# Kernel tuning notes

Hardware: AMD Instinct MI355X
Metric: run time of the kernel (lower is better)

## Reference

```python
import jax, jax.numpy as jnp
import numpy as np

B, N, D = 1, 2048, 512        # batch, query seq len, model dim
H, DH = 8, 64                 # heads, head dim
MEM = 512                     # cached XL memory tokens (one window segment)
KV = N + MEM                  # kv sequence length
WINDOW = 512                  # block / sliding-window size
LOOKBACK = 1                  # lookback_blocks
N_EP = 4                      # number of episodes
SCALE = DH ** -0.5


def _rope(t, pos):
    # t: [b,h,l,dh], pos: [l]  (GPT-NeoX half rotation)
    dh = t.shape[-1]
    inv_freq = 1.0 / (10000.0 ** (jnp.arange(0, dh, 2, dtype=jnp.float32) / dh))
    freqs = pos.astype(jnp.float32)[:, None] * inv_freq[None, :]   # [l, dh/2]
    freqs = jnp.concatenate([freqs, freqs], axis=-1)               # [l, dh]
    cos, sin = jnp.cos(freqs), jnp.sin(freqs)
    x1, x2 = jnp.split(t, 2, axis=-1)
    rotated = jnp.concatenate([-x2, x1], axis=-1)
    return t * cos + rotated * sin


def setup_inputs() -> dict:
    key = jax.random.key(0)
    ks = jax.random.split(key, 8)
    x = jax.random.normal(ks[0], (B, N, D), jnp.float32)
    cache_k = jax.random.normal(ks[1], (B, H, MEM, DH), jnp.float32)
    cache_v = jax.random.normal(ks[2], (B, H, MEM, DH), jnp.float32)
    episode_ids = jnp.sort(jax.random.randint(ks[3], (B, KV), 0, N_EP, dtype=jnp.int32), axis=-1)
    Wq = jax.random.normal(ks[4], (D, H * DH), jnp.float32) * 0.02
    Wkv = jax.random.normal(ks[5], (D, 2 * H * DH), jnp.float32) * 0.02
    Wg = jax.random.normal(ks[6], (D, H), jnp.float32) * 0.02
    Wo = jax.random.normal(ks[7], (H * DH, D), jnp.float32) * 0.02
    return dict(x=x, cache_k=cache_k, cache_v=cache_v, episode_ids=episode_ids,
                Wq=Wq, Wkv=Wkv, Wg=Wg, Wo=Wo)


def _xl_mask(episode_ids):
    # mirrors create_xl_mask: causal + block window with lookback + intra-episode
    offset = KV - N
    q_pos = offset + jnp.arange(N)          # [N]
    k_pos = jnp.arange(KV)                  # [KV]
    causal = q_pos[:, None] >= k_pos[None, :]
    bq = q_pos // WINDOW
    bk = k_pos // WINDOW
    block = (bq[:, None] >= bk[None, :]) & (bq[:, None] <= bk[None, :] + LOOKBACK)
    intra_ep = episode_ids[:, q_pos][:, :, None] == episode_ids[:, None, :]  # [B,N,KV]
    return (causal & block)[None] & intra_ep                                 # [B,N,KV]


def reference(x, cache_k, cache_v, episode_ids, Wq, Wkv, Wg, Wo):
    b, n, _ = x.shape
    offset = KV - N

    q = (x @ Wq).reshape(b, n, H, DH).transpose(0, 2, 1, 3)          # [b,h,n,dh]
    kv = (x @ Wkv).reshape(b, n, 2, H, DH)
    k_new = kv[:, :, 0].transpose(0, 2, 1, 3)                        # [b,h,n,dh]
    v_new = kv[:, :, 1].transpose(0, 2, 1, 3)

    k = jnp.concatenate([cache_k, k_new], axis=2)                    # [b,h,kv,dh]
    v = jnp.concatenate([cache_v, v_new], axis=2)

    q = _rope(q, offset + jnp.arange(n))
    k = _rope(k, jnp.arange(KV))

    scores = jnp.einsum('bhnd,bhmd->bhnm', q, k) * SCALE             # [b,h,n,kv]
    mask = _xl_mask(episode_ids)[:, None]                            # [b,1,n,kv]
    scores = jnp.where(mask, scores, jnp.finfo(scores.dtype).min)
    attn = jax.nn.softmax(scores, axis=-1)

    out = jnp.einsum('bhnm,bhmd->bhnd', attn, v)                     # [b,h,n,dh]

    gates = jax.nn.sigmoid(x @ Wg).transpose(0, 2, 1)[..., None]     # [b,h,n,1]
    out = out * gates

    out = out.transpose(0, 2, 1, 3).reshape(b, n, H * DH)            # merge heads
    return out @ Wo                                                  # [b,n,d]
```

## Files before the change

### kernel.cpp

```cpp
#include <hip/hip_runtime.h>
#include <math.h>

#define NQ     2048
#define DMODEL 512
#define NH     8
#define DHD    64
#define MEMT   512
#define KVT    2560
#define QSCALE 0.125f
#define NEGF   (-1e30f)

typedef unsigned short u16;
typedef __bf16 bf16x8 __attribute__((ext_vector_type(8)));
typedef float  f32x4  __attribute__((ext_vector_type(4)));
typedef u16    u16x8  __attribute__((ext_vector_type(8)));
typedef u16    u16x4  __attribute__((ext_vector_type(4)));

__device__ __forceinline__ u16 f2bf(float f) {
    union { float f; unsigned u; } v; v.f = f;
    unsigned r = (v.u + 0x7FFFu + ((v.u >> 16) & 1u)) >> 16;
    return (u16)r;
}

__global__ __launch_bounds__(256) void prep(const float* __restrict__ x,
                                            const float* __restrict__ Wq,
                                            const float* __restrict__ Wkv,
                                            const float* __restrict__ Wo,
                                            const float* __restrict__ Wg,
                                            const float* __restrict__ cache_v,
                                            u16* __restrict__ xb,
                                            u16* __restrict__ Wt,
                                            u16* __restrict__ Wot,
                                            float* __restrict__ gates,
                                            float2* __restrict__ cs,
                                            u16* __restrict__ vtb) {
    __shared__ __attribute__((aligned(16))) char smem[17408];
    int bid = blockIdx.x, tid = threadIdx.x;

    if (bid < 32) {
        int base4 = bid * 8192;
#pragma unroll
        for (int u = 0; u < 32; ++u) {
            int i4 = base4 + u * 256 + tid;
            float4 v = ((const float4*)x)[i4];
            u16x4 o4 = { f2bf(v.x), f2bf(v.y), f2bf(v.z), f2bf(v.w) };
            *(u16x4*)&xb[i4 * 4] = o4;
        }
    } else if (bid < 288) {
        float (*tile)[65] = (float(*)[65])smem;
        int tt = bid - 32;
        bool isQKV = (tt < 192);
        int tc, tr;
        if (isQKV) { tc = tt % 24; tr = tt / 24; }
        else       { tt -= 192; tc = tt & 7; tr = tt >> 3; }
        int rr = tid >> 4, c4 = (tid & 15) * 4;
#pragma unroll
        for (int u = 0; u < 4; ++u) {
            int row = u * 16 + rr;
            int k = tr * 64 + row, c = tc * 64 + c4;
            float4 v;
            if (isQKV) v = (c < 512) ? *(const float4*)&Wq[k * 512 + c]
                                     : *(const float4*)&Wkv[k * 1024 + (c - 512)];
            else       v = *(const float4*)&Wo[k * 512 + c];
            tile[row][c4 + 0] = v.x; tile[row][c4 + 1] = v.y;
            tile[row][c4 + 2] = v.z; tile[row][c4 + 3] = v.w;
        }
        __syncthreads();
#pragma unroll
        for (int u = 0; u < 4; ++u) {
            int trow = u * 16 + rr;
            u16x4 o4;
#pragma unroll
            for (int i = 0; i < 4; ++i) o4[i] = f2bf(tile[c4 + i][trow]);
            int tg = tc * 64 + trow, kg = tr * 64 + c4;
            if (isQKV) *(u16x4*)&Wt[tg * 512 + kg] = o4;
            else       *(u16x4*)&Wot[tg * 512 + kg] = o4;
        }
    } else if (bid < 320) {
#pragma unroll
        for (int kk = 0; kk < 2; ++kk) {
            int t = (bid - 288) * 512 + kk * 256 + tid;
            int n = t >> 3, hh = t & 7;
            float acc = 0.f;
            for (int k = 0; k < DMODEL; k += 4) {
                float4 xv = *(const float4*)&x[n * DMODEL + k];
                acc += xv.x * Wg[(k + 0) * NH + hh] + xv.y * Wg[(k + 1) * NH + hh]
                     + xv.z * Wg[(k + 2) * NH + hh] + xv.w * Wg[(k + 3) * NH + hh];
            }
            gates[hh * NQ + n] = 1.f / (1.f + __expf(-acc));
        }
    } else if (bid < 384) {
#pragma unroll
        for (int kk = 0; kk < 5; ++kk) {
            int idx = (bid - 320) * 1280 + kk * 256 + tid;
            int pos = idx >> 5, j = idx & 31;
            float invf = exp2f(-(float)j * (13.287712379549449f / 32.f));
            float ss, sc;
            sincosf((float)pos * invf, &ss, &sc);
            cs[idx] = make_float2(sc, ss);
        }
    } else {
        u16 (*tile)[66] = (u16(*)[66])smem;
        int uu = bid - 384;
        int tb = uu & 7, h = uu >> 3;
        int rr = tid >> 4, c4 = (tid & 15) * 4;
        int r0 = tb * 64;
#pragma unroll
        for (int u = 0; u < 4; ++u) {
            int row = u * 16 + rr;
            float4 v = *(const float4*)&cache_v[(h * MEMT + r0 + row) * DHD + c4];
            tile[row][c4 + 0] = f2bf(v.x); tile[row][c4 + 1] = f2bf(v.y);
            tile[row][c4 + 2] = f2bf(v.z); tile[row][c4 + 3] = f2bf(v.w);
        }
        __syncthreads();
#pragma unroll
        for (int u = 0; u < 4; ++u) {
            int d = u * 16 + rr;
            u16x4 o4 = { tile[c4 + 0][d], tile[c4 + 1][d], tile[c4 + 2][d], tile[c4 + 3][d] };
            *(u16x4*)&vtb[(h * DHD + d) * KVT + r0 + c4] = o4;
        }
    }
}

__global__ __launch_bounds__(256, 2) void qkv(const u16* __restrict__ xb,
                                              const u16* __restrict__ Wt,
                                              const float2* __restrict__ cs,
                                              const float* __restrict__ cache_k,
                                              u16* __restrict__ qb,
                                              u16* __restrict__ kb,
                                              u16* __restrict__ vtb) {
    __shared__ __attribute__((aligned(16))) u16 vtile[64][66];
    const int bid = blockIdx.x, tid = threadIdx.x;
    const int w = tid >> 6, lane = tid & 63;
    const int lr = lane & 15, lg = lane >> 4;

#pragma unroll 1
    for (int pass = 0; pass < 2; ++pass) {
        int u2 = pass * 512 + bid;
        if (u2 >= 832) break;
        if (u2 < 768) {
            int i = u2 >> 3;
            int bx = (u2 & 7) * 3 + (i >> 5);
            int by = i & 31;
            int rowbase = by * 64 + (w >> 1) * 32;
            int colbase = bx * 64 + (w & 1) * 16;
            f32x4 acc[2][2];
#pragma unroll
            for (int a = 0; a < 2; ++a)
#pragma unroll
                for (int b = 0; b < 2; ++b) { f32x4 z = {0.f,0.f,0.f,0.f}; acc[a][b] = z; }
            const u16* a0 = xb + (rowbase + lr) * 512 + lg * 8;
            const u16* a1 = a0 + 16 * 512;
            const u16* b0 = Wt + (colbase + lr) * 512 + lg * 8;
            const u16* b1 = b0 + 32 * 512;
#pragma unroll 4
            for (int k0 = 0; k0 < 512; k0 += 32) {
                bf16x8 fa0 = __builtin_bit_cast(bf16x8, *(const u16x8*)(a0 + k0));
                bf16x8 fa1 = __builtin_bit_cast(bf16x8, *(const u16x8*)(a1 + k0));
                bf16x8 fb0 = __builtin_bit_cast(bf16x8, *(const u16x8*)(b0 + k0));
                bf16x8 fb1 = __builtin_bit_cast(bf16x8, *(const u16x8*)(b1 + k0));
                acc[0][0] = __builtin_amdgcn_mfma_f32_16x16x32_bf16(fa0, fb0, acc[0][0], 0, 0, 0);
                acc[0][1] = __builtin_amdgcn_mfma_f32_16x16x32_bf16(fa0, fb1, acc[0][1], 0, 0, 0);
                acc[1][0] = __builtin_amdgcn_mfma_f32_16x16x32_bf16(fa1, fb0, acc[1][0], 0, 0, 0);
                acc[1][1] = __builtin_amdgcn_mfma_f32_16x16x32_bf16(fa1, fb1, acc[1][1], 0, 0, 0);
            }
            int j = (colbase & 63) + lr;
            int region = bx >> 3;
            int h = bx & 7;
            if (region == 2) {
                __syncthreads();
#pragma unroll
                for (int rt = 0; rt < 2; ++rt)
#pragma unroll
                    for (int r = 0; r < 4; ++r) {
                        int rl = (w >> 1) * 32 + rt * 16 + lg * 4 + r;
                        vtile[rl][j]      = f2bf(acc[rt][0][r]);
                        vtile[rl][j + 32] = f2bf(acc[rt][1][r]);
                    }
                __syncthreads();
                int rr = tid >> 4, c4 = (tid & 15) * 4;
#pragma unroll
                for (int u = 0; u < 4; ++u) {
                    int d = u * 16 + rr;
                    u16x4 o4 = { vtile[c4 + 0][d], vtile[c4 + 1][d], vtile[c4 + 2][d], vtile[c4 + 3][d] };
                    *(u16x4*)&vtb[(h * DHD + d) * KVT + 512 + by * 64 + c4] = o4;
                }
            } else {
#pragma unroll
                for (int rt = 0; rt < 2; ++rt)
#pragma unroll
                    for (int r = 0; r < 4; ++r) {
                        int n = rowbase + rt * 16 + lg * 4 + r;
                        float a = acc[rt][0][r], b = acc[rt][1][r];
                        float2 csv = cs[(512 + n) * 32 + j];
                        u16 e0 = f2bf(a * csv.x - b * csv.y);
                        u16 e1 = f2bf(b * csv.x + a * csv.y);
                        if (region == 0) {
                            qb[(h * NQ + n) * DHD + j]      = e0;
                            qb[(h * NQ + n) * DHD + 32 + j] = e1;
                        } else {
                            kb[(h * KVT + 512 + n) * DHD + j]      = e0;
                            kb[(h * KVT + 512 + n) * DHD + 32 + j] = e1;
                        }
                    }
            }
        } else {
            int uu = u2 - 768;
            int r0 = (uu & 7) * 64, h = uu >> 3;
#pragma unroll
            for (int u = 0; u < 8; ++u) {
                int idx = u * 256 + tid;
                int row = idx >> 5, j = idx & 31;
                int r = r0 + row;
                float a = cache_k[(h * MEMT + r) * DHD + j];
                float b = cache_k[(h * MEMT + r) * DHD + 32 + j];
                float2 csv = cs[r * 32 + j];
                kb[(h * KVT + r) * DHD + j]      = f2bf(a * csv.x - b * csv.y);
                kb[(h * KVT + r) * DHD + 32 + j] = f2bf(b * csv.x + a * csv.y);
            }
        }
    }
}

#define LOADK(BK, BEP, C0)                                                     \
  _Pragma("unroll")                                                            \
  for (int t = 0; t < 4; ++t) {                                                \
    const u16* kr = kb + ((h * KVT + (C0) + t * 16 + lr) * DHD + lg * 8);      \
    BK[t][0] = __builtin_bit_cast(bf16x8, *(const u16x8*)kr);                  \
    BK[t][1] = __builtin_bit_cast(bf16x8, *(const u16x8*)(kr + 32));           \
    BEP[t] = ep[(C0) + t * 16 + lr];                                           \
  }

#define DO_CHUNK(C0, BK, BEP, PREF, NBK, NBEP)                                 \
  {                                                                            \
    bf16x8 bV[4][2];                                                           \
    _Pragma("unroll")                                                          \
    for (int t = 0; t < 4; ++t) {                                              \
      const u16* vr = vtb + ((h * DHD + t * 16 + lr) * KVT + (C0) + lg * 8);   \
      bV[t][0] = __builtin_bit_cast(bf16x8, *(const u16x8*)vr);                \
      bV[t][1] = __builtin_bit_cast(bf16x8, *(const u16x8*)(vr + 32));         \
    }                                                                          \
    f32x4 s[4];                                                                \
    _Pragma("unroll")                                                          \
    for (int t = 0; t < 4; ++t) {                                              \
      f32x4 z = {0.f, 0.f, 0.f, 0.f};                                          \
      s[t] = __builtin_amdgcn_mfma_f32_16x16x32_bf16(aQ[0], BK[t][0], z, 0, 0, 0); \
      s[t] = __builtin_amdgcn_mfma_f32_16x16x32_bf16(aQ[1], BK[t][1], s[t], 0, 0, 0); \
    }                                                                          \
    if (PREF) { LOADK(NBK, NBEP, (C0) + 64) }                                  \
    float rmax[4] = {NEGF, NEGF, NEGF, NEGF};                                  \
    _Pragma("unroll")                                                          \
    for (int t = 0; t < 4; ++t) {                                              \
      int key = (C0) + t * 16 + lr;                                            \
      int ek = BEP[t];                                                         \
      _Pragma("unroll")                                                        \
      for (int r = 0; r < 4; ++r) {                                            \
        bool vld = (key <= qpos[r]) && (ek == epq[r]);                         \
        float sv = vld ? s[t][r] * QSCALE : NEGF;                              \
        s[t][r] = sv;                                                          \
        rmax[r] = fmaxf(rmax[r], sv);                                          \
      }                                                                        \
    }                                                                          \
    _Pragma("unroll")                                                          \
    for (int mm = 1; mm < 16; mm <<= 1) {                                      \
      _Pragma("unroll")                                                        \
      for (int r = 0; r < 4; ++r)                                              \
        rmax[r] = fmaxf(rmax[r], __shfl_xor(rmax[r], mm, 64));                 \
    }                                                                          \
    float alpha[4];                                                            \
    _Pragma("unroll")                                                          \
    for (int r = 0; r < 4; ++r) {                                              \
      float mn = fmaxf(mrun[r], rmax[r]);                                      \
      alpha[r] = __expf(mrun[r] - mn);                                         \
      mrun[r] = mn;                                                            \
      lsum[r] *= alpha[r];                                                     \
    }                                                                          \
    _Pragma("unroll")                                                          \
    for (int t = 0; t < 4; ++t)                                                \
      _Pragma("unroll")                                                        \
      for (int r = 0; r < 4; ++r) o[t][r] *= alpha[r];                         \
    float psum[4] = {0.f, 0.f, 0.f, 0.f};                                      \
    _Pragma("unroll")                                                          \
    for (int t = 0; t < 4; ++t) {                                              \
      _Pragma("unroll")                                                        \
      for (int r = 0; r < 4; ++r) {                                            \
        float sv = s[t][r];                                                    \
        float p = (sv <= -1e29f) ? 0.f : __expf(sv - mrun[r]);                 \
        psum[r] += p;                                                          \
        int qq = lg * 4 + r;                                                   \
        int kk2 = t * 16 + lr;                                                 \
        pl[qq * 64 + (kk2 ^ ((qq & 7) << 3))] = f2bf(p);                       \
      }                                                                        \
    }                                                                          \
    _Pragma("unroll")                                                          \
    for (int mm = 1; mm < 16; mm <<= 1) {                                      \
      _Pragma("unroll")                                                        \
      for (int r = 0; r < 4; ++r) psum[r] += __shfl_xor(psum[r], mm, 64);      \
    }                                                                          \
    _Pragma("unroll")                                                          \
    for (int r = 0; r < 4; ++r) lsum[r] += psum[r];                            \
    bf16x8 aP[2];                                                              \
    {                                                                          \
      int sw = (lr & 7) << 3;                                                  \
      aP[0] = __builtin_bit_cast(bf16x8, *(const u16x8*)&pl[lr * 64 + ((lg * 8) ^ sw)]);        \
      aP[1] = __builtin_bit_cast(bf16x8, *(const u16x8*)&pl[lr * 64 + ((32 + lg * 8) ^ sw)]);   \
    }                                                                          \
    _Pragma("unroll")                                                          \
    for (int t = 0; t < 4; ++t) {                                              \
      o[t] = __builtin_amdgcn_mfma_f32_16x16x32_bf16(aP[0], bV[t][0], o[t], 0, 0, 0); \
      o[t] = __builtin_amdgcn_mfma_f32_16x16x32_bf16(aP[1], bV[t][1], o[t], 0, 0, 0); \
    }                                                                          \
  }

__global__ __launch_bounds__(256, 2) void attn_mfma(const u16* __restrict__ qb,
                                                    const u16* __restrict__ kb,
                                                    const u16* __restrict__ vtb,
                                                    const float* __restrict__ gates,
                                                    const int* __restrict__ ep,
                                                    u16* __restrict__ outp) {
    __shared__ u16 plds[4][16 * 64];
    __shared__ float o_l[2][16][68];
    __shared__ float ml_l[2][2][16];

    int bid = blockIdx.x;
    int h = bid & 7;
    int q0 = (bid >> 3) * 32;
    int tid = threadIdx.x;
    int w = tid >> 6, lane = tid & 63;
    int lr = lane & 15, lg = lane >> 4;
    int qsub = w & 1, kvh = w >> 1;
    int qbase = q0 + qsub * 16;
    u16* pl = plds[w];

    bf16x8 aQ[2];
    {
        const u16* qrow = qb + ((h * NQ + qbase + lr) * DHD + lg * 8);
        aQ[0] = __builtin_bit_cast(bf16x8, *(const u16x8*)qrow);
        aQ[1] = __builtin_bit_cast(bf16x8, *(const u16x8*)(qrow + 32));
    }

    int qpos[4], epq[4];
    float gq[4];
#pragma unroll
    for (int r = 0; r < 4; ++r) {
        int q = qbase + lg * 4 + r;
        qpos[r] = 512 + q;
        epq[r] = ep[512 + q];
        gq[r] = gates[h * NQ + q];
    }

    f32x4 o[4];
    float mrun[4], lsum[4];
#pragma unroll
    for (int t = 0; t < 4; ++t) { f32x4 z = {0.f,0.f,0.f,0.f}; o[t] = z; }
#pragma unroll
    for (int r = 0; r < 4; ++r) { mrun[r] = NEGF; lsum[r] = 0.f; }

    int c_lo = q0 & ~511;
    int nch = (544 + (q0 & 511) + 63) >> 6;
    int n0 = nch >> 1;
    int my_n = kvh ? (nch - n0) : n0;
    int c0 = c_lo + (kvh ? (n0 << 6) : 0);

    bf16x8 bKA[4][2], bKB[4][2];
    int epA[4], epB[4];

    LOADK(bKA, epA, c0)
    int ci = 0;
    while (true) {
        bool more = (ci + 1 < my_n);
        DO_CHUNK(c0, bKA, epA, more, bKB, epB)
        ++ci; c0 += 64;
        if (!more) break;
        bool more2 = (ci + 1 < my_n);
        DO_CHUNK(c0, bKB, epB, more2, bKA, epA)
        ++ci; c0 += 64;
        if (!more2) break;
    }

    if (kvh == 1) {
#pragma unroll
        for (int r = 0; r < 4; ++r) {
            ml_l[qsub][0][lg * 4 + r] = mrun[r];
            ml_l[qsub][1][lg * 4 + r] = lsum[r];
        }
#pragma unroll
        for (int t = 0; t < 4; ++t)
#pragma unroll
            for (int r = 0; r < 4; ++r)
                o_l[qsub][lg * 4 + r][t * 16 + lr] = o[t][r];
    }
    __syncthreads();
    if (kvh == 0) {
#pragma unroll
        for (int r = 0; r < 4; ++r) {
            int row = lg * 4 + r;
            float m1 = ml_l[qsub][0][row], l1 = ml_l[qsub][1][row];
            float m0 = mrun[r], l0 = lsum[r];
            float mm2 = fmaxf(m0, m1);
            float f0 = (m0 <= -1e29f) ? 0.f : __expf(m0 - mm2);
            float f1 = (m1 <= -1e29f) ? 0.f : __expf(m1 - mm2);
            float lt = l0 * f0 + l1 * f1;
            float inv = gq[r] / lt;
            int q = qbase + row;
#pragma unroll
            for (int t = 0; t < 4; ++t) {
                float o1 = o_l[qsub][row][t * 16 + lr];
                outp[q * DMODEL + h * DHD + t * 16 + lr] =
                    f2bf((o[t][r] * f0 + o1 * f1) * inv);
            }
        }
    }
}

__global__ __launch_bounds__(256, 2) void outgemm(const u16* __restrict__ attnb,
                                                  const u16* __restrict__ Wot,
                                                  float* __restrict__ outf) {
    int bid = blockIdx.x, tid = threadIdx.x;
    int w = tid >> 6, lane = tid & 63;
    int lr = lane & 15, lg = lane >> 4;
    int bx = bid & 7, by = bid >> 3;
    int rowbase = by * 32 + (w >> 1) * 16;
    int colbase = bx * 64 + (w & 1) * 16;
    f32x4 acc0 = {0.f,0.f,0.f,0.f}, acc1 = {0.f,0.f,0.f,0.f};
    const u16* a0 = attnb + (rowbase + lr) * 512 + lg * 8;
    const u16* b0 = Wot + (colbase + lr) * 512 + lg * 8;
    const u16* b1 = b0 + 32 * 512;
#pragma unroll 4
    for (int k0 = 0; k0 < 512; k0 += 32) {
        bf16x8 fa  = __builtin_bit_cast(bf16x8, *(const u16x8*)(a0 + k0));
        bf16x8 fb0 = __builtin_bit_cast(bf16x8, *(const u16x8*)(b0 + k0));
        bf16x8 fb1 = __builtin_bit_cast(bf16x8, *(const u16x8*)(b1 + k0));
        acc0 = __builtin_amdgcn_mfma_f32_16x16x32_bf16(fa, fb0, acc0, 0, 0, 0);
        acc1 = __builtin_amdgcn_mfma_f32_16x16x32_bf16(fa, fb1, acc1, 0, 0, 0);
    }
#pragma unroll
    for (int r = 0; r < 4; ++r) {
        int n = rowbase + lg * 4 + r;
        outf[n * DMODEL + colbase + lr]      = acc0[r];
        outf[n * DMODEL + colbase + 32 + lr] = acc1[r];
    }
}

extern "C" void kernel_launch(void* const* d_in, const int* in_sizes, int n_in,
                              void* d_out, int out_size, void* d_ws, size_t ws_size,
                              hipStream_t stream) {
    const float* x       = (const float*)d_in[0];
    const float* cache_k = (const float*)d_in[1];
    const float* cache_v = (const float*)d_in[2];
    const int*   ep      = (const int*)  d_in[3];
    const float* Wq      = (const float*)d_in[4];
    const float* Wkv     = (const float*)d_in[5];
    const float* Wg      = (const float*)d_in[6];
    const float* Wo      = (const float*)d_in[7];
    float* out = (float*)d_out;

    u16* u = (u16*)d_ws;
    u16* x_bf    = u;
    u16* Wt      = x_bf + 1048576;
    u16* Wot     = Wt + 786432;
    u16* q_bf    = Wot + 262144;
    u16* k_bf    = q_bf + 1048576;
    u16* vT      = k_bf + 1310720;
    u16* attn_bf = vT + 1310720;
    float*  gatesw = (float*)(attn_bf + 1048576);
    float2* cs     = (float2*)(gatesw + 16384);

    prep<<<448, 256, 0, stream>>>(x, Wq, Wkv, Wo, Wg, cache_v, x_bf, Wt, Wot, gatesw, cs, vT);
    qkv<<<512, 256, 0, stream>>>(x_bf, Wt, cs, cache_k, q_bf, k_bf, vT);
    attn_mfma<<<512, 256, 0, stream>>>(q_bf, k_bf, vT, gatesw, ep, attn_bf);
    outgemm<<<512, 256, 0, stream>>>(attn_bf, Wot, out);
}
```

Before: 159.6 us.

## Shrink per-block work to launch more blocks across all four kernels

Moves the cache_k RoPE work into the prep kernel, computing sin/cos inline. Each remaining kernel is split finer: qkv runs 32-row tiles over 1536 blocks, attention uses 16 query rows per block with the KV range split four ways across waves, and the output GEMM uses 16-row tiles over 1024 blocks. Launch bounds rise to 4 blocks per CU. The goal is to fill the large GPU with more concurrent blocks and waves. In exchange it adds a 4-way softmax merge through shared memory and less register-level reuse per wave in the GEMMs.

Result: slower. 212.0 us (+32.8%).

```diff
diff --git a/kernel.cpp b/kernel.cpp
--- a/kernel.cpp
+++ b/kernel.cpp
@@ -15,6 +15,7 @@
 typedef float  f32x4  __attribute__((ext_vector_type(4)));
 typedef u16    u16x8  __attribute__((ext_vector_type(8)));
 typedef u16    u16x4  __attribute__((ext_vector_type(4)));
+typedef u16    u16x2  __attribute__((ext_vector_type(2)));
 
 __device__ __forceinline__ u16 f2bf(float f) {
     union { float f; unsigned u; } v; v.f = f;
@@ -22,19 +23,21 @@
     return (u16)r;
 }
 
-__global__ __launch_bounds__(256) void prep(const float* __restrict__ x,
-                                            const float* __restrict__ Wq,
-                                            const float* __restrict__ Wkv,
-                                            const float* __restrict__ Wo,
-                                            const float* __restrict__ Wg,
-                                            const float* __restrict__ cache_v,
-                                            u16* __restrict__ xb,
-                                            u16* __restrict__ Wt,
-                                            u16* __restrict__ Wot,
-                                            float* __restrict__ gates,
-                                            float2* __restrict__ cs,
-                                            u16* __restrict__ vtb) {
-    __shared__ __attribute__((aligned(16))) char smem[17408];
+__global__ __launch_bounds__(256, 4) void prep(const float* __restrict__ x,
+                                               const float* __restrict__ Wq,
+                                               const float* __restrict__ Wkv,
+                                               const float* __restrict__ Wo,
+                                               const float* __restrict__ Wg,
+                                               const float* __restrict__ cache_v,
+                                               const float* __restrict__ cache_k,
+                                               u16* __restrict__ xb,
+                                               u16* __restrict__ Wt,
+                                               u16* __restrict__ Wot,
+                                               float* __restrict__ gates,
+                                               float2* __restrict__ cs,
+                                               u16* __restrict__ vtb,
+                                               u16* __restrict__ kb) {
+    __shared__ __attribute__((aligned(16))) char smem[16640];
     int bid = blockIdx.x, tid = threadIdx.x;
 
     if (bid < 32) {
@@ -99,7 +102,7 @@
             sincosf((float)pos * invf, &ss, &sc);
             cs[idx] = make_float2(sc, ss);
         }
-    } else {
+    } else if (bid < 448) {
         u16 (*tile)[66] = (u16(*)[66])smem;
         int uu = bid - 384;
         int tb = uu & 7, h = uu >> 3;
@@ -119,104 +122,90 @@
             u16x4 o4 = { tile[c4 + 0][d], tile[c4 + 1][d], tile[c4 + 2][d], tile[c4 + 3][d] };
             *(u16x4*)&vtb[(h * DHD + d) * KVT + r0 + c4] = o4;
         }
-    }
-}
-
-__global__ __launch_bounds__(256, 2) void qkv(const u16* __restrict__ xb,
+    } else {
+        int uu = bid - 448;
+        int r0 = (uu & 7) * 64, h = uu >> 3;
+        int j = tid & 31;
+        float invf = exp2f(-(float)j * (13.287712379549449f / 32.f));
+#pragma unroll
+        for (int u = 0; u < 8; ++u) {
+            int idx = u * 256 + tid;
+            int row = idx >> 5;
+            int r = r0 + row;
+            float a = cache_k[(h * MEMT + r) * DHD + j];
+            float b = cache_k[(h * MEMT + r) * DHD + 32 + j];
+            float ss, sc;
+            sincosf((float)r * invf, &ss, &sc);
+            kb[(h * KVT + r) * DHD + j]      = f2bf(a * sc - b * ss);
+            kb[(h * KVT + r) * DHD + 32 + j] = f2bf(b * sc + a * ss);
+        }
+    }
+}
+
+__global__ __launch_bounds__(256, 4) void qkv(const u16* __restrict__ xb,
                                               const u16* __restrict__ Wt,
                                               const float2* __restrict__ cs,
-                                              const float* __restrict__ cache_k,
                                               u16* __restrict__ qb,
                                               u16* __restrict__ kb,
                                               u16* __restrict__ vtb) {
-    __shared__ __attribute__((aligned(16))) u16 vtile[64][66];
+    __shared__ __attribute__((aligned(16))) u16 vtile[32][66];
     const int bid = blockIdx.x, tid = threadIdx.x;
     const int w = tid >> 6, lane = tid & 63;
     const int lr = lane & 15, lg = lane >> 4;
 
-#pragma unroll 1
-    for (int pass = 0; pass < 2; ++pass) {
-        int u2 = pass * 512 + bid;
-        if (u2 >= 832) break;
-        if (u2 < 768) {
-            int i = u2 >> 3;
-            int bx = (u2 & 7) * 3 + (i >> 5);
-            int by = i & 31;
-            int rowbase = by * 64 + (w >> 1) * 32;
-            int colbase = bx * 64 + (w & 1) * 16;
-            f32x4 acc[2][2];
-#pragma unroll
-            for (int a = 0; a < 2; ++a)
-#pragma unroll
-                for (int b = 0; b < 2; ++b) { f32x4 z = {0.f,0.f,0.f,0.f}; acc[a][b] = z; }
-            const u16* a0 = xb + (rowbase + lr) * 512 + lg * 8;
-            const u16* a1 = a0 + 16 * 512;
-            const u16* b0 = Wt + (colbase + lr) * 512 + lg * 8;
-            const u16* b1 = b0 + 32 * 512;
+    int i = bid >> 3;
+    int sub = i % 3, byr = i / 3;
+    int bx = (bid & 7) * 3 + sub;
+    int rowbase = byr * 32;
+    int rfrag = rowbase + (w >> 1) * 16;
+    int colbase = bx * 64 + (w & 1) * 16;
+
+    f32x4 acc0 = {0.f,0.f,0.f,0.f}, acc1 = {0.f,0.f,0.f,0.f};
+    const u16* a0 = xb + (rfrag + lr) * 512 + lg * 8;
+    const u16* b0 = Wt + (colbase + lr) * 512 + lg * 8;
+    const u16* b1 = b0 + 32 * 512;
 #pragma unroll 4
-            for (int k0 = 0; k0 < 512; k0 += 32) {
-                bf16x8 fa0 = __builtin_bit_cast(bf16x8, *(const u16x8*)(a0 + k0));
-                bf16x8 fa1 = __builtin_bit_cast(bf16x8, *(const u16x8*)(a1 + k0));
-                bf16x8 fb0 = __builtin_bit_cast(bf16x8, *(const u16x8*)(b0 + k0));
-                bf16x8 fb1 = __builtin_bit_cast(bf16x8, *(const u16x8*)(b1 + k0));
-                acc[0][0] = __builtin_amdgcn_mfma_f32_16x16x32_bf16(fa0, fb0, acc[0][0], 0, 0, 0);
-                acc[0][1] = __builtin_amdgcn_mfma_f32_16x16x32_bf16(fa0, fb1, acc[0][1], 0, 0, 0);
-                acc[1][0] = __builtin_amdgcn_mfma_f32_16x16x32_bf16(fa1, fb0, acc[1][0], 0, 0, 0);
-                acc[1][1] = __builtin_amdgcn_mfma_f32_16x16x32_bf16(fa1, fb1, acc[1][1], 0, 0, 0);
-            }
-            int j = (colbase & 63) + lr;
-            int region = bx >> 3;
-            int h = bx & 7;
-            if (region == 2) {
-                __syncthreads();
-#pragma unroll
-                for (int rt = 0; rt < 2; ++rt)
-#pragma unroll
-                    for (int r = 0; r < 4; ++r) {
-                        int rl = (w >> 1) * 32 + rt * 16 + lg * 4 + r;
-                        vtile[rl][j]      = f2bf(acc[rt][0][r]);
-                        vtile[rl][j + 32] = f2bf(acc[rt][1][r]);
-                    }
-                __syncthreads();
-                int rr = tid >> 4, c4 = (tid & 15) * 4;
-#pragma unroll
-                for (int u = 0; u < 4; ++u) {
-                    int d = u * 16 + rr;
-                    u16x4 o4 = { vtile[c4 + 0][d], vtile[c4 + 1][d], vtile[c4 + 2][d], vtile[c4 + 3][d] };
-                    *(u16x4*)&vtb[(h * DHD + d) * KVT + 512 + by * 64 + c4] = o4;
-                }
+    for (int k0 = 0; k0 < 512; k0 += 32) {
+        bf16x8 fa  = __builtin_bit_cast(bf16x8, *(const u16x8*)(a0 + k0));
+        bf16x8 fb0 = __builtin_bit_cast(bf16x8, *(const u16x8*)(b0 + k0));
+        bf16x8 fb1 = __builtin_bit_cast(bf16x8, *(const u16x8*)(b1 + k0));
+        acc0 = __builtin_amdgcn_mfma_f32_16x16x32_bf16(fa, fb0, acc0, 0, 0, 0);
+        acc1 = __builtin_amdgcn_mfma_f32_16x16x32_bf16(fa, fb1, acc1, 0, 0, 0);
+    }
+
+    int j = (colbase & 63) + lr;
+    int region = bx >> 3;
+    int h = bx & 7;
+    if (region == 2) {
+        __syncthreads();
+#pragma unroll
+        for (int r = 0; r < 4; ++r) {
+            int rl = (w >> 1) * 16 + lg * 4 + r;
+            vtile[rl][j]      = f2bf(acc0[r]);
+            vtile[rl][j + 32] = f2bf(acc1[r]);
+        }
+        __syncthreads();
+        int rr = tid >> 4, c2 = (tid & 15) * 2;
+#pragma unroll
+        for (int u = 0; u < 4; ++u) {
+            int d = u * 16 + rr;
+            u16x2 o2 = { vtile[c2][d], vtile[c2 + 1][d] };
+            *(u16x2*)&vtb[(h * DHD + d) * KVT + 512 + rowbase + c2] = o2;
+        }
+    } else {
+#pragma unroll
+        for (int r = 0; r < 4; ++r) {
+            int n = rfrag + lg * 4 + r;
+            float a = acc0[r], b = acc1[r];
+            float2 csv = cs[(512 + n) * 32 + j];
+            u16 e0 = f2bf(a * csv.x - b * csv.y);
+            u16 e1 = f2bf(b * csv.x + a * csv.y);
+            if (region == 0) {
+                qb[(h * NQ + n) * DHD + j]      = e0;
+                qb[(h * NQ + n) * DHD + 32 + j] = e1;
             } else {
-#pragma unroll
-                for (int rt = 0; rt < 2; ++rt)
-#pragma unroll
-                    for (int r = 0; r < 4; ++r) {
-                        int n = rowbase + rt * 16 + lg * 4 + r;
-                        float a = acc[rt][0][r], b = acc[rt][1][r];
-                        float2 csv = cs[(512 + n) * 32 + j];
-                        u16 e0 = f2bf(a * csv.x - b * csv.y);
-                        u16 e1 = f2bf(b * csv.x + a * csv.y);
-                        if (region == 0) {
-                            qb[(h * NQ + n) * DHD + j]      = e0;
-                            qb[(h * NQ + n) * DHD + 32 + j] = e1;
-                        } else {
-                            kb[(h * KVT + 512 + n) * DHD + j]      = e0;
-                            kb[(h * KVT + 512 + n) * DHD + 32 + j] = e1;
-                        }
-                    }
-            }
-        } else {
-            int uu = u2 - 768;
-            int r0 = (uu & 7) * 64, h = uu >> 3;
-#pragma unroll
-            for (int u = 0; u < 8; ++u) {
-                int idx = u * 256 + tid;
-                int row = idx >> 5, j = idx & 31;
-                int r = r0 + row;
-                float a = cache_k[(h * MEMT + r) * DHD + j];
-                float b = cache_k[(h * MEMT + r) * DHD + 32 + j];
-                float2 csv = cs[r * 32 + j];
-                kb[(h * KVT + r) * DHD + j]      = f2bf(a * csv.x - b * csv.y);
-                kb[(h * KVT + r) * DHD + 32 + j] = f2bf(b * csv.x + a * csv.y);
+                kb[(h * KVT + 512 + n) * DHD + j]      = e0;
+                kb[(h * KVT + 512 + n) * DHD + 32 + j] = e1;
             }
         }
     }
@@ -312,29 +301,27 @@
     }                                                                          \
   }
 
-__global__ __launch_bounds__(256, 2) void attn_mfma(const u16* __restrict__ qb,
+__global__ __launch_bounds__(256, 4) void attn_mfma(const u16* __restrict__ qb,
                                                     const u16* __restrict__ kb,
                                                     const u16* __restrict__ vtb,
                                                     const float* __restrict__ gates,
                                                     const int* __restrict__ ep,
                                                     u16* __restrict__ outp) {
-    __shared__ u16 plds[4][16 * 64];
-    __shared__ float o_l[2][16][68];
-    __shared__ float ml_l[2][2][16];
+    __shared__ u16 plds[4][1024];
+    __shared__ float o_l[4][16][68];
+    __shared__ float ml_l[4][2][16];
 
     int bid = blockIdx.x;
     int h = bid & 7;
-    int q0 = (bid >> 3) * 32;
+    int q0 = (bid >> 3) * 16;
     int tid = threadIdx.x;
     int w = tid >> 6, lane = tid & 63;
     int lr = lane & 15, lg = lane >> 4;
-    int qsub = w & 1, kvh = w >> 1;
-    int qbase = q0 + qsub * 16;
     u16* pl = plds[w];
 
     bf16x8 aQ[2];
     {
-        const u16* qrow = qb + ((h * NQ + qbase + lr) * DHD + lg * 8);
+        const u16* qrow = qb + ((h * NQ + q0 + lr) * DHD + lg * 8);
         aQ[0] = __builtin_bit_cast(bf16x8, *(const u16x8*)qrow);
         aQ[1] = __builtin_bit_cast(bf16x8, *(const u16x8*)(qrow + 32));
     }
@@ -343,7 +330,7 @@
     float gq[4];
 #pragma unroll
     for (int r = 0; r < 4; ++r) {
-        int q = qbase + lg * 4 + r;
+        int q = q0 + lg * 4 + r;
         qpos[r] = 512 + q;
         epq[r] = ep[512 + q];
         gq[r] = gates[h * NQ + q];
@@ -357,10 +344,11 @@
     for (int r = 0; r < 4; ++r) { mrun[r] = NEGF; lsum[r] = 0.f; }
 
     int c_lo = q0 & ~511;
-    int nch = (544 + (q0 & 511) + 63) >> 6;
-    int n0 = nch >> 1;
-    int my_n = kvh ? (nch - n0) : n0;
-    int c0 = c_lo + (kvh ? (n0 << 6) : 0);
+    int nch = (591 + (q0 & 511)) >> 6;
+    int base = nch >> 2, rem = nch & 3;
+    int my_n = base + (w < rem ? 1 : 0);
+    int pre = w * base + (w < rem ? w : rem);
+    int c0 = c_lo + (pre << 6);
 
     bf16x8 bKA[4][2], bKB[4][2];
     int epA[4], epB[4];
@@ -378,67 +366,65 @@
         if (!more2) break;
     }
 
-    if (kvh == 1) {
-#pragma unroll
-        for (int r = 0; r < 4; ++r) {
-            ml_l[qsub][0][lg * 4 + r] = mrun[r];
-            ml_l[qsub][1][lg * 4 + r] = lsum[r];
-        }
-#pragma unroll
-        for (int t = 0; t < 4; ++t)
-#pragma unroll
-            for (int r = 0; r < 4; ++r)
-                o_l[qsub][lg * 4 + r][t * 16 + lr] = o[t][r];
-    }
-    __syncthreads();
-    if (kvh == 0) {
+    if (lr == 0) {
 #pragma unroll
         for (int r = 0; r < 4; ++r) {
             int row = lg * 4 + r;
-            float m1 = ml_l[qsub][0][row], l1 = ml_l[qsub][1][row];
-            float m0 = mrun[r], l0 = lsum[r];
-            float mm2 = fmaxf(m0, m1);
-            float f0 = (m0 <= -1e29f) ? 0.f : __expf(m0 - mm2);
-            float f1 = (m1 <= -1e29f) ? 0.f : __expf(m1 - mm2);
-            float lt = l0 * f0 + l1 * f1;
-            float inv = gq[r] / lt;
-            int q = qbase + row;
-#pragma unroll
-            for (int t = 0; t < 4; ++t) {
-                float o1 = o_l[qsub][row][t * 16 + lr];
-                outp[q * DMODEL + h * DHD + t * 16 + lr] =
-                    f2bf((o[t][r] * f0 + o1 * f1) * inv);
-            }
-        }
-    }
-}
-
-__global__ __launch_bounds__(256, 2) void outgemm(const u16* __restrict__ attnb,
+            ml_l[w][0][row] = mrun[r];
+            ml_l[w][1][row] = lsum[r];
+        }
+    }
+    __syncthreads();
+    float inv[4];
+#pragma unroll
+    for (int r = 0; r < 4; ++r) {
+        int row = lg * 4 + r;
+        float mg = NEGF;
+#pragma unroll
+        for (int s = 0; s < 4; ++s) mg = fmaxf(mg, ml_l[s][0][row]);
+        float lt = 0.f;
+#pragma unroll
+        for (int s = 0; s < 4; ++s) {
+            float ms = ml_l[s][0][row];
+            if (ms > -1e29f) lt += ml_l[s][1][row] * __expf(ms - mg);
+        }
+        float f = (mrun[r] > -1e29f) ? __expf(mrun[r] - mg) : 0.f;
+#pragma unroll
+        for (int t = 0; t < 4; ++t) o_l[w][row][t * 16 + lr] = o[t][r] * f;
+        inv[r] = gq[r] / lt;
+    }
+    __syncthreads();
+#pragma unroll
+    for (int r = 0; r < 4; ++r) {
+        int row = lg * 4 + r;
+        float sum = o_l[0][row][w * 16 + lr] + o_l[1][row][w * 16 + lr]
+                  + o_l[2][row][w * 16 + lr] + o_l[3][row][w * 16 + lr];
+        outp[(q0 + row) * DMODEL + h * DHD + w * 16 + lr] = f2bf(sum * inv[r]);
+    }
+}
+
+__global__ __launch_bounds__(256, 4) void outgemm(const u16* __restrict__ attnb,
                                                   const u16* __restrict__ Wot,
                                                   float* __restrict__ outf) {
     int bid = blockIdx.x, tid = threadIdx.x;
     int w = tid >> 6, lane = tid & 63;
     int lr = lane & 15, lg = lane >> 4;
     int bx = bid & 7, by = bid >> 3;
-    int rowbase = by * 32 + (w >> 1) * 16;
-    int colbase = bx * 64 + (w & 1) * 16;
-    f32x4 acc0 = {0.f,0.f,0.f,0.f}, acc1 = {0.f,0.f,0.f,0.f};
+    int rowbase = by * 16;
+    int colbase = bx * 64 + w * 16;
+    f32x4 acc = {0.f,0.f,0.f,0.f};
     const u16* a0 = attnb + (rowbase + lr) * 512 + lg * 8;
     const u16* b0 = Wot + (colbase + lr) * 512 + lg * 8;
-    const u16* b1 = b0 + 32 * 512;
 #pragma unroll 4
     for (int k0 = 0; k0 < 512; k0 += 32) {
-        bf16x8 fa  = __builtin_bit_cast(bf16x8, *(const u16x8*)(a0 + k0));
-        bf16x8 fb0 = __builtin_bit_cast(bf16x8, *(const u16x8*)(b0 + k0));
-        bf16x8 fb1 = __builtin_bit_cast(bf16x8, *(const u16x8*)(b1 + k0));
-        acc0 = __builtin_amdgcn_mfma_f32_16x16x32_bf16(fa, fb0, acc0, 0, 0, 0);
-        acc1 = __builtin_amdgcn_mfma_f32_16x16x32_bf16(fa, fb1, acc1, 0, 0, 0);
+        bf16x8 fa = __builtin_bit_cast(bf16x8, *(const u16x8*)(a0 + k0));
+        bf16x8 fb = __builtin_bit_cast(bf16x8, *(const u16x8*)(b0 + k0));
+        acc = __builtin_amdgcn_mfma_f32_16x16x32_bf16(fa, fb, acc, 0, 0, 0);
     }
 #pragma unroll
     for (int r = 0; r < 4; ++r) {
         int n = rowbase + lg * 4 + r;
-        outf[n * DMODEL + colbase + lr]      = acc0[r];
-        outf[n * DMODEL + colbase + 32 + lr] = acc1[r];
+        outf[n * DMODEL + colbase + lr] = acc[r];
     }
 }
 
@@ -466,8 +452,9 @@
     float*  gatesw = (float*)(attn_bf + 1048576);
     float2* cs     = (float2*)(gatesw + 16384);
 
-    prep<<<448, 256, 0, stream>>>(x, Wq, Wkv, Wo, Wg, cache_v, x_bf, Wt, Wot, gatesw, cs, vT);
-    qkv<<<512, 256, 0, stream>>>(x_bf, Wt, cs, cache_k, q_bf, k_bf, vT);
-    attn_mfma<<<512, 256, 0, stream>>>(q_bf, k_bf, vT, gatesw, ep, attn_bf);
-    outgemm<<<512, 256, 0, stream>>>(attn_bf, Wot, out);
-}
+    prep<<<512, 256, 0, stream>>>(x, Wq, Wkv, Wo, Wg, cache_v, cache_k,
+                                  x_bf, Wt, Wot, gatesw, cs, vT, k_bf);
+    qkv<<<1536, 256, 0, stream>>>(x_bf, Wt, cs, q_bf, k_bf, vT);
+    attn_mfma<<<1024, 256, 0, stream>>>(q_bf, k_bf, vT, gatesw, ep, attn_bf);
+    outgemm<<<1024, 256, 0, stream>>>(attn_bf, Wot, out);
+}
```
